# Optimization experiments

Hardware: AMD Instinct MI355X
Metric: run time of the kernel (lower is better)

## Reference

```python
import jax, jax.numpy as jnp
import numpy as np

EPS = 1e-5
HEADS, DIM_HEAD = 8, 64


def rmsnorm(x, g):
    # einn.Norm('b... [d]', mean=False, bias=False): rms-normalize last dim, learned scale
    return x * jax.lax.rsqrt(jnp.mean(jnp.square(x), axis=-1, keepdims=True) + EPS) * g


def setup_inputs() -> dict:
    key = jax.random.key(0)
    ks = jax.random.split(key, 10)
    B, N, D, DE, H, DH = 1, 1024, 512, 64, HEADS, DIM_HEAD
    s = 0.02
    return {
        'x': jax.random.normal(ks[0], (B, N, D), jnp.float32),
        'mask': jnp.ones((B, N), dtype=bool),
        'edges': jax.random.normal(ks[1], (B, N, N, DE), jnp.float32),
        'rms_g': jnp.ones((D,), jnp.float32),
        'w_qkv': jax.random.normal(ks[2], (D, 3 * H * DH), jnp.float32) * s,
        'w_gates': jax.random.normal(ks[3], (D, H), jnp.float32) * s,
        'b_gates': jnp.zeros((H,), jnp.float32),
        'edges_rms_g': jnp.ones((DE,), jnp.float32),
        'w_eb': jax.random.normal(ks[4], (DE, H), jnp.float32) * s,
        'b_eb': jnp.zeros((H,), jnp.float32),
        'w_th': jnp.eye(H, dtype=jnp.float32) + jax.random.normal(ks[5], (H, H), jnp.float32) * s,
        'w_out': jax.random.normal(ks[6], (H * DH, D), jnp.float32) * s,
        'w_eout': jax.random.normal(ks[7], (H, DE), jnp.float32) * s,
    }


def reference(x, mask, edges, rms_g, w_qkv, w_gates, b_gates, edges_rms_g, w_eb, b_eb, w_th, w_out, w_eout):
    B, N, D = x.shape
    H, DH = HEADS, DIM_HEAD
    scale = DH ** 0.5  # NOTE: source multiplies q by dim_head**0.5 (faithful)

    xn = rmsnorm(x, rms_g)
    qkv = (xn @ w_qkv).reshape(B, N, 3, H, DH)
    q = jnp.transpose(qkv[:, :, 0], (0, 2, 1, 3)) * scale  # b h n d
    k = jnp.transpose(qkv[:, :, 1], (0, 2, 1, 3))
    v = jnp.transpose(qkv[:, :, 2], (0, 2, 1, 3))

    sim = jnp.einsum('bhid,bhjd->bhij', q, k)
    # edge bias: rmsnorm -> Linear(dim_edges, heads) -> b h i j
    bias = jnp.einsum('bije,eh->bhij', rmsnorm(edges, edges_rms_g), w_eb) + b_eb[None, :, None, None]
    sim = sim + bias
    # pre talking heads: Conv2d(H, H, 1, bias=False)
    sim = jnp.einsum('bhij,gh->bgij', sim, w_th)

    mask_value = -jnp.finfo(sim.dtype).max
    sim = jnp.where(mask[:, None, None, :], sim, mask_value)

    attn = jax.nn.softmax(sim, axis=-1)
    out = jnp.einsum('bhij,bhjd->bhid', attn, v)

    gates = jax.nn.sigmoid(xn @ w_gates + b_gates)  # b n h
    out = out * jnp.transpose(gates, (0, 2, 1))[..., None]  # b h n 1

    out = jnp.transpose(out, (0, 2, 1, 3)).reshape(B, N, H * DH) @ w_out  # b n dim
    edges_out = jnp.einsum('bhij,he->bije', attn, w_eout)  # Conv2d(H, DE, 1) then b d i j -> b i j d
    return out, edges_out
```

## Files before the change

kernel.cpp:

```cpp
#include <hip/hip_runtime.h>
#include <math.h>

#define EPS 1e-5f

__global__ __launch_bounds__(256) void prep_kernel(
    const float* __restrict__ w_th, const float* __restrict__ w_eb,
    const float* __restrict__ b_eb, const float* __restrict__ erg,
    float* __restrict__ G2, float* __restrict__ b2)
{
  int t = threadIdx.x;
  for (int idx = t; idx < 512; idx += 256) {
    int g = idx >> 6, d = idx & 63;
    float s = 0.f;
#pragma unroll
    for (int h = 0; h < 8; ++h) s += w_th[g * 8 + h] * w_eb[d * 8 + h];
    G2[idx] = erg[d] * s;
  }
  if (t < 8) {
    float s = 0.f;
#pragma unroll
    for (int h = 0; h < 8; ++h) s += w_th[t * 8 + h] * b_eb[h];
    b2[t] = s;
  }
}

__global__ __launch_bounds__(256) void rms_gates_kernel(
    const float* __restrict__ x, const float* __restrict__ rms_g,
    const float* __restrict__ w_gates, const float* __restrict__ b_gates,
    float* __restrict__ xn, float* __restrict__ gates)
{
  int i = blockIdx.x, t = threadIdx.x;
  __shared__ float red[4][9];
  float2 v = *(const float2*)&x[i * 512 + t * 2];
  float g0 = rms_g[t * 2], g1 = rms_g[t * 2 + 1];
  float a0 = v.x * g0, a1 = v.y * g1;
  float ssq = v.x * v.x + v.y * v.y;
  float4 wa = *(const float4*)&w_gates[t * 16 + 0];
  float4 wb = *(const float4*)&w_gates[t * 16 + 4];
  float4 wc = *(const float4*)&w_gates[t * 16 + 8];
  float4 wd = *(const float4*)&w_gates[t * 16 + 12];
  float ph[8];
  ph[0] = a0 * wa.x + a1 * wc.x; ph[1] = a0 * wa.y + a1 * wc.y;
  ph[2] = a0 * wa.z + a1 * wc.z; ph[3] = a0 * wa.w + a1 * wc.w;
  ph[4] = a0 * wb.x + a1 * wd.x; ph[5] = a0 * wb.y + a1 * wd.y;
  ph[6] = a0 * wb.z + a1 * wd.z; ph[7] = a0 * wb.w + a1 * wd.w;
#pragma unroll
  for (int off = 32; off >= 1; off >>= 1) {
    ssq += __shfl_xor(ssq, off, 64);
#pragma unroll
    for (int h = 0; h < 8; ++h) ph[h] += __shfl_xor(ph[h], off, 64);
  }
  int wv = t >> 6;
  if ((t & 63) == 0) {
    red[wv][0] = ssq;
#pragma unroll
    for (int h = 0; h < 8; ++h) red[wv][1 + h] = ph[h];
  }
  __syncthreads();
  float ssqT = red[0][0] + red[1][0] + red[2][0] + red[3][0];
  float inv = rsqrtf(ssqT * (1.0f / 512.0f) + EPS);
  float2 o; o.x = v.x * inv * g0; o.y = v.y * inv * g1;
  *(float2*)&xn[i * 512 + t * 2] = o;
  if (t < 8) {
    float p = red[0][1 + t] + red[1][1 + t] + red[2][1 + t] + red[3][1 + t];
    float z = p * inv + b_gates[t];
    gates[i * 8 + t] = 1.0f / (1.0f + __expf(-z));
  }
}

__global__ __launch_bounds__(256) void gemm32_f32(
    const float* __restrict__ A, const float* __restrict__ B, float* __restrict__ C,
    int M, int N, int K)
{
  __shared__ float As[16][40];
  __shared__ float Bs[16][68];
  int t = threadIdx.x;
  int row0 = blockIdx.y * 32, col0 = blockIdx.x * 64;
  int tm = t & 7, tn = t >> 3;
  int ar = t >> 2, ac = (t & 3) * 4;
  int br = t >> 4, bc = (t & 15) * 4;
  float4 av, bv;
  if (t < 128) av = *(const float4*)&A[(size_t)(row0 + ar) * K + ac];
  bv = *(const float4*)&B[(size_t)br * N + col0 + bc];
  float acc[4][2] = {};
  for (int k0 = 0; k0 < K; k0 += 16) {
    __syncthreads();
    if (t < 128) {
      As[ac + 0][ar] = av.x; As[ac + 1][ar] = av.y; As[ac + 2][ar] = av.z; As[ac + 3][ar] = av.w;
    }
    *(float4*)&Bs[br][bc] = bv;
    __syncthreads();
    if (k0 + 16 < K) {
      if (t < 128) av = *(const float4*)&A[(size_t)(row0 + ar) * K + k0 + 16 + ac];
      bv = *(const float4*)&B[(size_t)(k0 + 16 + br) * N + col0 + bc];
    }
#pragma unroll
    for (int k = 0; k < 16; ++k) {
      float4 a = *(const float4*)&As[k][tm * 4];
      float2 b = *(const float2*)&Bs[k][tn * 2];
      acc[0][0] += a.x * b.x; acc[0][1] += a.x * b.y;
      acc[1][0] += a.y * b.x; acc[1][1] += a.y * b.y;
      acc[2][0] += a.z * b.x; acc[2][1] += a.z * b.y;
      acc[3][0] += a.w * b.x; acc[3][1] += a.w * b.y;
    }
  }
#pragma unroll
  for (int aa = 0; aa < 4; ++aa) {
    float2 o; o.x = acc[aa][0]; o.y = acc[aa][1];
    *(float2*)&C[(size_t)(row0 + tm * 4 + aa) * N + col0 + tn * 2] = o;
  }
}

__global__ __launch_bounds__(256) void qk_kernel(
    const float* __restrict__ qkv, float* __restrict__ sim)
{
  int jt = blockIdx.x, it = blockIdx.y, h = blockIdx.z;
  __shared__ float Qs[16][68];
  __shared__ float Ks[16][68];
  int t = threadIdx.x;
  int tm = t & 15, tn = t >> 4;
  int r = t >> 2, c4 = (t & 3) * 4;
  const float* qb = qkv + h * 64;
  const float* kb = qkv + 512 + h * 64;
  float4 qv = *(const float4*)&qb[(size_t)(it * 64 + r) * 1536 + c4];
  float4 kv = *(const float4*)&kb[(size_t)(jt * 64 + r) * 1536 + c4];
  float acc[4][4] = {};
  for (int k0 = 0; k0 < 64; k0 += 16) {
    __syncthreads();
    Qs[c4 + 0][r] = qv.x * 8.0f; Qs[c4 + 1][r] = qv.y * 8.0f; Qs[c4 + 2][r] = qv.z * 8.0f; Qs[c4 + 3][r] = qv.w * 8.0f;
    Ks[c4 + 0][r] = kv.x; Ks[c4 + 1][r] = kv.y; Ks[c4 + 2][r] = kv.z; Ks[c4 + 3][r] = kv.w;
    __syncthreads();
    if (k0 + 16 < 64) {
      qv = *(const float4*)&qb[(size_t)(it * 64 + r) * 1536 + k0 + 16 + c4];
      kv = *(const float4*)&kb[(size_t)(jt * 64 + r) * 1536 + k0 + 16 + c4];
    }
#pragma unroll
    for (int k = 0; k < 16; ++k) {
      float4 a = *(const float4*)&Qs[k][tm * 4];
      float4 b = *(const float4*)&Ks[k][tn * 4];
      acc[0][0] += a.x * b.x; acc[0][1] += a.x * b.y; acc[0][2] += a.x * b.z; acc[0][3] += a.x * b.w;
      acc[1][0] += a.y * b.x; acc[1][1] += a.y * b.y; acc[1][2] += a.y * b.z; acc[1][3] += a.y * b.w;
      acc[2][0] += a.z * b.x; acc[2][1] += a.z * b.y; acc[2][2] += a.z * b.z; acc[2][3] += a.z * b.w;
      acc[3][0] += a.w * b.x; acc[3][1] += a.w * b.y; acc[3][2] += a.w * b.z; acc[3][3] += a.w * b.w;
    }
  }
#pragma unroll
  for (int aa = 0; aa < 4; ++aa) {
    float4 o; o.x = acc[aa][0]; o.y = acc[aa][1]; o.z = acc[aa][2]; o.w = acc[aa][3];
    *(float4*)&sim[((size_t)h << 20) + (size_t)(it * 64 + tm * 4 + aa) * 1024 + jt * 64 + tn * 4] = o;
  }
}

__global__ __launch_bounds__(256) void attn_fused2(
    float* __restrict__ simattn,
    const float* __restrict__ edges,
    const float* __restrict__ w_th,
    const float* __restrict__ G2,
    const float* __restrict__ b2,
    const float* __restrict__ w_eout,
    float* __restrict__ edges_out)
{
  __shared__ float tile[256 * 17];
  __shared__ float red[4][8];
  int i = blockIdx.x, t = threadIdx.x;
  int wv = t >> 6;
  int sub = t & 15, grp = t >> 4;

  float weo[8][4];
#pragma unroll
  for (int g = 0; g < 8; ++g) {
    float4 v = *(const float4*)&w_eout[g * 64 + sub * 4];
    weo[g][0] = v.x; weo[g][1] = v.y; weo[g][2] = v.z; weo[g][3] = v.w;
  }
  float b2r[8];
#pragma unroll
  for (int g = 0; g < 8; ++g) b2r[g] = b2[g];

  const float* erow = edges + (size_t)i * 65536;
  float lgv[4][8];
  float vmax[8];
#pragma unroll
  for (int g = 0; g < 8; ++g) vmax[g] = -1e30f;

  float4 pf[4];
#pragma unroll
  for (int it = 0; it < 4; ++it) {
    int jr = (t >> 2) + 64 * it;
    pf[it] = *(const float4*)&erow[(size_t)jr * 64 + (t & 3) * 4];
  }

  for (int jg = 0; jg < 4; ++jg) {
    float ssq = 0.f;
    float dot[8] = {0.f, 0.f, 0.f, 0.f, 0.f, 0.f, 0.f, 0.f};
    for (int dc = 0; dc < 4; ++dc) {
      __syncthreads();
#pragma unroll
      for (int it = 0; it < 4; ++it) {
        int jr = (t >> 2) + 64 * it;
        float4 v = pf[it];
        tile[jr * 17 + (t & 3) * 4 + 0] = v.x;
        tile[jr * 17 + (t & 3) * 4 + 1] = v.y;
        tile[jr * 17 + (t & 3) * 4 + 2] = v.z;
        tile[jr * 17 + (t & 3) * 4 + 3] = v.w;
      }
      __syncthreads();
      {
        int ndc = dc + 1, njg = jg;
        if (ndc == 4) { ndc = 0; ++njg; }
        if (njg < 4) {
#pragma unroll
          for (int it = 0; it < 4; ++it) {
            int jr = (t >> 2) + 64 * it;
            pf[it] = *(const float4*)&erow[(size_t)(njg * 256 + jr) * 64 + ndc * 16 + (t & 3) * 4];
          }
        }
      }
#pragma unroll
      for (int d = 0; d < 16; ++d) {
        float e = tile[t * 17 + d];
        ssq += e * e;
        int dd = dc * 16 + d;
#pragma unroll
        for (int g = 0; g < 8; ++g) dot[g] += e * G2[g * 64 + dd];
      }
    }
    int j = jg * 256 + t;
    float l[8];
#pragma unroll
    for (int h = 0; h < 8; ++h) l[h] = simattn[((size_t)h << 20) + ((size_t)i << 10) + j];
    float r = rsqrtf(ssq * (1.0f / 64.0f) + EPS);
#pragma unroll
    for (int g = 0; g < 8; ++g) {
      float s = 0.f;
#pragma unroll
      for (int h = 0; h < 8; ++h) s += w_th[g * 8 + h] * l[h];
      s += dot[g] * r + b2r[g];
      lgv[jg][g] = s;
      vmax[g] = fmaxf(vmax[g], s);
    }
  }
#pragma unroll
  for (int g = 0; g < 8; ++g) {
#pragma unroll
    for (int off = 32; off >= 1; off >>= 1) vmax[g] = fmaxf(vmax[g], __shfl_xor(vmax[g], off, 64));
  }
  if ((t & 63) == 0) {
#pragma unroll
    for (int g = 0; g < 8; ++g) red[wv][g] = vmax[g];
  }
  __syncthreads();
  float mx[8];
#pragma unroll
  for (int g = 0; g < 8; ++g)
    mx[g] = fmaxf(fmaxf(red[0][g], red[1][g]), fmaxf(red[2][g], red[3][g]));
  __syncthreads();
  float vsum[8] = {0.f, 0.f, 0.f, 0.f, 0.f, 0.f, 0.f, 0.f};
#pragma unroll
  for (int jg = 0; jg < 4; ++jg) {
#pragma unroll
    for (int g = 0; g < 8; ++g) {
      float ev = __expf(lgv[jg][g] - mx[g]);
      lgv[jg][g] = ev;
      vsum[g] += ev;
    }
  }
#pragma unroll
  for (int g = 0; g < 8; ++g) {
#pragma unroll
    for (int off = 32; off >= 1; off >>= 1) vsum[g] += __shfl_xor(vsum[g], off, 64);
  }
  if ((t & 63) == 0) {
#pragma unroll
    for (int g = 0; g < 8; ++g) red[wv][g] = vsum[g];
  }
  __syncthreads();
  float inv[8];
#pragma unroll
  for (int g = 0; g < 8; ++g)
    inv[g] = 1.0f / (red[0][g] + red[1][g] + red[2][g] + red[3][g]);
#pragma unroll
  for (int jg = 0; jg < 4; ++jg) {
    int j = jg * 256 + t;
#pragma unroll
    for (int g = 0; g < 8; ++g) {
      float a = lgv[jg][g] * inv[g];
      lgv[jg][g] = a;
      simattn[((size_t)g << 20) + ((size_t)i << 10) + j] = a;
    }
  }
  float* lgc = tile;
  for (int jg = 0; jg < 4; ++jg) {
    __syncthreads();
#pragma unroll
    for (int g = 0; g < 8; ++g) lgc[g * 256 + t] = lgv[jg][g];
    __syncthreads();
#pragma unroll
    for (int pass = 0; pass < 16; ++pass) {
      int jj = pass * 16 + grp;
      float a[8];
#pragma unroll
      for (int g = 0; g < 8; ++g) a[g] = lgc[g * 256 + jj];
      float4 o;
      o.x = a[0] * weo[0][0]; o.y = a[0] * weo[0][1]; o.z = a[0] * weo[0][2]; o.w = a[0] * weo[0][3];
#pragma unroll
      for (int g = 1; g < 8; ++g) {
        o.x += a[g] * weo[g][0]; o.y += a[g] * weo[g][1];
        o.z += a[g] * weo[g][2]; o.w += a[g] * weo[g][3];
      }
      *(float4*)&edges_out[((size_t)(i * 1024 + jg * 256 + jj)) * 64 + sub * 4] = o;
    }
  }
}

__global__ __launch_bounds__(256) void av_kernel(
    const float* __restrict__ attn, const float* __restrict__ qkv,
    const float* __restrict__ gates, float* __restrict__ outh)
{
  int it = blockIdx.y, g = blockIdx.z;
  __shared__ float As[16][40];
  __shared__ float Bs[16][68];
  int t = threadIdx.x;
  int tm = t & 7, tn = t >> 3;
  int ar = t >> 2, ac = (t & 3) * 4;
  int br = t >> 4, bc = (t & 15) * 4;
  const float* Ab = attn + ((size_t)g << 20) + (size_t)(it * 32) * 1024;
  const float* Bb = qkv + 1024 + g * 64;
  float4 av, bv;
  if (t < 128) av = *(const float4*)&Ab[(size_t)ar * 1024 + ac];
  bv = *(const float4*)&Bb[(size_t)br * 1536 + bc];
  float acc[4][2] = {};
  for (int k0 = 0; k0 < 1024; k0 += 16) {
    __syncthreads();
    if (t < 128) {
      As[ac + 0][ar] = av.x; As[ac + 1][ar] = av.y; As[ac + 2][ar] = av.z; As[ac + 3][ar] = av.w;
    }
    *(float4*)&Bs[br][bc] = bv;
    __syncthreads();
    if (k0 + 16 < 1024) {
      if (t < 128) av = *(const float4*)&Ab[(size_t)ar * 1024 + k0 + 16 + ac];
      bv = *(const float4*)&Bb[(size_t)(k0 + 16 + br) * 1536 + bc];
    }
#pragma unroll
    for (int k = 0; k < 16; ++k) {
      float4 a = *(const float4*)&As[k][tm * 4];
      float2 b = *(const float2*)&Bs[k][tn * 2];
      acc[0][0] += a.x * b.x; acc[0][1] += a.x * b.y;
      acc[1][0] += a.y * b.x; acc[1][1] += a.y * b.y;
      acc[2][0] += a.z * b.x; acc[2][1] += a.z * b.y;
      acc[3][0] += a.w * b.x; acc[3][1] += a.w * b.y;
    }
  }
#pragma unroll
  for (int aa = 0; aa < 4; ++aa) {
    int irow = it * 32 + tm * 4 + aa;
    float gt = gates[irow * 8 + g];
    float2 o; o.x = acc[aa][0] * gt; o.y = acc[aa][1] * gt;
    *(float2*)&outh[(size_t)irow * 512 + g * 64 + tn * 2] = o;
  }
}

extern "C" void kernel_launch(void* const* d_in, const int* in_sizes, int n_in,
                              void* d_out, int out_size, void* d_ws, size_t ws_size,
                              hipStream_t stream) {
  const float* x       = (const float*)d_in[0];
  const float* edges   = (const float*)d_in[2];
  const float* rms_g   = (const float*)d_in[3];
  const float* w_qkv   = (const float*)d_in[4];
  const float* w_gates = (const float*)d_in[5];
  const float* b_gates = (const float*)d_in[6];
  const float* erg     = (const float*)d_in[7];
  const float* w_eb    = (const float*)d_in[8];
  const float* b_eb    = (const float*)d_in[9];
  const float* w_th    = (const float*)d_in[10];
  const float* w_out   = (const float*)d_in[11];
  const float* w_eout  = (const float*)d_in[12];

  float* out = (float*)d_out;
  float* eo  = out + 1024 * 512;

  float* ws    = (float*)d_ws;
  float* xn    = ws;
  float* gates = xn + 524288;
  float* qkv   = gates + 8192;
  float* sim   = qkv + 1572864;
  float* outh  = sim + 8388608;
  float* G2    = outh + 524288;
  float* b2    = G2 + 512;

  prep_kernel<<<1, 256, 0, stream>>>(w_th, w_eb, b_eb, erg, G2, b2);
  rms_gates_kernel<<<1024, 256, 0, stream>>>(x, rms_g, w_gates, b_gates, xn, gates);
  gemm32_f32<<<dim3(1536 / 64, 1024 / 32), 256, 0, stream>>>(xn, w_qkv, qkv, 1024, 1536, 512);
  qk_kernel<<<dim3(16, 16, 8), 256, 0, stream>>>(qkv, sim);
  attn_fused2<<<1024, 256, 0, stream>>>(sim, edges, w_th, G2, b2, w_eout, eo);
  av_kernel<<<dim3(1, 32, 8), 256, 0, stream>>>(sim, qkv, gates, outh);
  gemm32_f32<<<dim3(512 / 64, 1024 / 32), 256, 0, stream>>>(outh, w_out, out, 1024, 512, 512);
}
```

Measured before the change: 625.1 us.

## Split attn-V GEMM over key chunks, add 64x64 QKV GEMM, single-stage QK tile

The attention-times-V kernel previously launched only 256 blocks, each looping over all 1024 keys. It is now split into 8 key chunks that write partial sums to a workspace, followed by a reduction kernel that sums the partials and applies the sigmoid gates. The QKV projection switches to a new 64x64-tile GEMM, which gives more reuse per block but launches fewer blocks. The QK kernel now loads the full 64-wide head dimension into shared memory at once, removing the inner sync loop. In exchange this adds an extra partial-sum buffer, one more launch, and larger shared-memory use in the QK kernel.

```diff
diff --git a/kernel.cpp b/kernel.cpp
--- a/kernel.cpp
+++ b/kernel.cpp
@@ -111,38 +111,81 @@
   }
 }
 
+__global__ __launch_bounds__(256) void gemm64_f32(
+    const float* __restrict__ A, const float* __restrict__ B, float* __restrict__ C,
+    int M, int N, int K)
+{
+  __shared__ float As[16][68];
+  __shared__ float Bs[16][68];
+  int t = threadIdx.x;
+  int row0 = blockIdx.y * 64, col0 = blockIdx.x * 64;
+  int tm = t & 15, tn = t >> 4;
+  int ar = t >> 2, ac = (t & 3) * 4;
+  int br = t >> 4, bc = (t & 15) * 4;
+  float4 av = *(const float4*)&A[(size_t)(row0 + ar) * K + ac];
+  float4 bv = *(const float4*)&B[(size_t)br * N + col0 + bc];
+  float acc[4][4] = {};
+  for (int k0 = 0; k0 < K; k0 += 16) {
+    __syncthreads();
+    As[ac + 0][ar] = av.x; As[ac + 1][ar] = av.y; As[ac + 2][ar] = av.z; As[ac + 3][ar] = av.w;
+    *(float4*)&Bs[br][bc] = bv;
+    __syncthreads();
+    if (k0 + 16 < K) {
+      av = *(const float4*)&A[(size_t)(row0 + ar) * K + k0 + 16 + ac];
+      bv = *(const float4*)&B[(size_t)(k0 + 16 + br) * N + col0 + bc];
+    }
+#pragma unroll
+    for (int k = 0; k < 16; ++k) {
+      float4 a = *(const float4*)&As[k][tn * 4];
+      float4 b = *(const float4*)&Bs[k][tm * 4];
+      acc[0][0] += a.x * b.x; acc[0][1] += a.x * b.y; acc[0][2] += a.x * b.z; acc[0][3] += a.x * b.w;
+      acc[1][0] += a.y * b.x; acc[1][1] += a.y * b.y; acc[1][2] += a.y * b.z; acc[1][3] += a.y * b.w;
+      acc[2][0] += a.z * b.x; acc[2][1] += a.z * b.y; acc[2][2] += a.z * b.z; acc[2][3] += a.z * b.w;
+      acc[3][0] += a.w * b.x; acc[3][1] += a.w * b.y; acc[3][2] += a.w * b.z; acc[3][3] += a.w * b.w;
+    }
+  }
+#pragma unroll
+  for (int r = 0; r < 4; ++r) {
+    float4 o; o.x = acc[r][0]; o.y = acc[r][1]; o.z = acc[r][2]; o.w = acc[r][3];
+    *(float4*)&C[(size_t)(row0 + tn * 4 + r) * N + col0 + tm * 4] = o;
+  }
+}
+
 __global__ __launch_bounds__(256) void qk_kernel(
     const float* __restrict__ qkv, float* __restrict__ sim)
 {
   int jt = blockIdx.x, it = blockIdx.y, h = blockIdx.z;
-  __shared__ float Qs[16][68];
-  __shared__ float Ks[16][68];
+  __shared__ float Qs[64][68];
+  __shared__ float Ks[64][68];
   int t = threadIdx.x;
   int tm = t & 15, tn = t >> 4;
   int r = t >> 2, c4 = (t & 3) * 4;
   const float* qb = qkv + h * 64;
   const float* kb = qkv + 512 + h * 64;
-  float4 qv = *(const float4*)&qb[(size_t)(it * 64 + r) * 1536 + c4];
-  float4 kv = *(const float4*)&kb[(size_t)(jt * 64 + r) * 1536 + c4];
+  float4 qv[4], kv[4];
+#pragma unroll
+  for (int ch = 0; ch < 4; ++ch) {
+    qv[ch] = *(const float4*)&qb[(size_t)(it * 64 + r) * 1536 + ch * 16 + c4];
+    kv[ch] = *(const float4*)&kb[(size_t)(jt * 64 + r) * 1536 + ch * 16 + c4];
+  }
+#pragma unroll
+  for (int ch = 0; ch < 4; ++ch) {
+    int d0 = ch * 16 + c4;
+    Qs[d0 + 0][r] = qv[ch].x * 8.0f; Qs[d0 + 1][r] = qv[ch].y * 8.0f;
+    Qs[d0 + 2][r] = qv[ch].z * 8.0f; Qs[d0 + 3][r] = qv[ch].w * 8.0f;
+    Ks[d0 + 0][r] = kv[ch].x; Ks[d0 + 1][r] = kv[ch].y;
+    Ks[d0 + 2][r] = kv[ch].z; Ks[d0 + 3][r] = kv[ch].w;
+  }
+  __syncthreads();
   float acc[4][4] = {};
-  for (int k0 = 0; k0 < 64; k0 += 16) {
-    __syncthreads();
-    Qs[c4 + 0][r] = qv.x * 8.0f; Qs[c4 + 1][r] = qv.y * 8.0f; Qs[c4 + 2][r] = qv.z * 8.0f; Qs[c4 + 3][r] = qv.w * 8.0f;
-    Ks[c4 + 0][r] = kv.x; Ks[c4 + 1][r] = kv.y; Ks[c4 + 2][r] = kv.z; Ks[c4 + 3][r] = kv.w;
-    __syncthreads();
-    if (k0 + 16 < 64) {
-      qv = *(const float4*)&qb[(size_t)(it * 64 + r) * 1536 + k0 + 16 + c4];
-      kv = *(const float4*)&kb[(size_t)(jt * 64 + r) * 1536 + k0 + 16 + c4];
-    }
-#pragma unroll
-    for (int k = 0; k < 16; ++k) {
-      float4 a = *(const float4*)&Qs[k][tm * 4];
-      float4 b = *(const float4*)&Ks[k][tn * 4];
-      acc[0][0] += a.x * b.x; acc[0][1] += a.x * b.y; acc[0][2] += a.x * b.z; acc[0][3] += a.x * b.w;
-      acc[1][0] += a.y * b.x; acc[1][1] += a.y * b.y; acc[1][2] += a.y * b.z; acc[1][3] += a.y * b.w;
-      acc[2][0] += a.z * b.x; acc[2][1] += a.z * b.y; acc[2][2] += a.z * b.z; acc[2][3] += a.z * b.w;
-      acc[3][0] += a.w * b.x; acc[3][1] += a.w * b.y; acc[3][2] += a.w * b.z; acc[3][3] += a.w * b.w;
-    }
+#pragma unroll
+  for (int k = 0; k < 64; ++k) {
+    float4 a = *(const float4*)&Qs[k][tm * 4];
+    float4 b = *(const float4*)&Ks[k][tn * 4];
+    acc[0][0] += a.x * b.x; acc[0][1] += a.x * b.y; acc[0][2] += a.x * b.z; acc[0][3] += a.x * b.w;
+    acc[1][0] += a.y * b.x; acc[1][1] += a.y * b.y; acc[1][2] += a.y * b.z; acc[1][3] += a.y * b.w;
+    acc[2][0] += a.z * b.x; acc[2][1] += a.z * b.y; acc[2][2] += a.z * b.z; acc[2][3] += a.z * b.w;
+    acc[3][0] += a.w * b.x; acc[3][1] += a.w * b.y; acc[3][2] += a.w * b.z; acc[3][3] += a.w * b.w;
   }
 #pragma unroll
   for (int aa = 0; aa < 4; ++aa) {
@@ -312,31 +355,31 @@
   }
 }
 
-__global__ __launch_bounds__(256) void av_kernel(
+__global__ __launch_bounds__(256) void av_part(
     const float* __restrict__ attn, const float* __restrict__ qkv,
-    const float* __restrict__ gates, float* __restrict__ outh)
-{
-  int it = blockIdx.y, g = blockIdx.z;
+    float* __restrict__ outp)
+{
+  int jc = blockIdx.x, it = blockIdx.y, g = blockIdx.z;
   __shared__ float As[16][40];
   __shared__ float Bs[16][68];
   int t = threadIdx.x;
   int tm = t & 7, tn = t >> 3;
   int ar = t >> 2, ac = (t & 3) * 4;
   int br = t >> 4, bc = (t & 15) * 4;
-  const float* Ab = attn + ((size_t)g << 20) + (size_t)(it * 32) * 1024;
-  const float* Bb = qkv + 1024 + g * 64;
+  const float* Ab = attn + ((size_t)g << 20) + (size_t)(it * 32) * 1024 + jc * 128;
+  const float* Bb = qkv + 1024 + g * 64 + (size_t)(jc * 128) * 1536;
   float4 av, bv;
   if (t < 128) av = *(const float4*)&Ab[(size_t)ar * 1024 + ac];
   bv = *(const float4*)&Bb[(size_t)br * 1536 + bc];
   float acc[4][2] = {};
-  for (int k0 = 0; k0 < 1024; k0 += 16) {
+  for (int k0 = 0; k0 < 128; k0 += 16) {
     __syncthreads();
     if (t < 128) {
       As[ac + 0][ar] = av.x; As[ac + 1][ar] = av.y; As[ac + 2][ar] = av.z; As[ac + 3][ar] = av.w;
     }
     *(float4*)&Bs[br][bc] = bv;
     __syncthreads();
-    if (k0 + 16 < 1024) {
+    if (k0 + 16 < 128) {
       if (t < 128) av = *(const float4*)&Ab[(size_t)ar * 1024 + k0 + 16 + ac];
       bv = *(const float4*)&Bb[(size_t)(k0 + 16 + br) * 1536 + bc];
     }
@@ -353,10 +396,26 @@
 #pragma unroll
   for (int aa = 0; aa < 4; ++aa) {
     int irow = it * 32 + tm * 4 + aa;
-    float gt = gates[irow * 8 + g];
-    float2 o; o.x = acc[aa][0] * gt; o.y = acc[aa][1] * gt;
-    *(float2*)&outh[(size_t)irow * 512 + g * 64 + tn * 2] = o;
-  }
+    float2 o; o.x = acc[aa][0]; o.y = acc[aa][1];
+    *(float2*)&outp[((size_t)jc * 1024 + irow) * 512 + g * 64 + tn * 2] = o;
+  }
+}
+
+__global__ __launch_bounds__(256) void av_reduce(
+    const float* __restrict__ outp, const float* __restrict__ gates,
+    float* __restrict__ outh)
+{
+  int i = blockIdx.x, t = threadIdx.x;
+  int c = t * 2;
+  float2 s = *(const float2*)&outp[(size_t)i * 512 + c];
+#pragma unroll
+  for (int jc = 1; jc < 8; ++jc) {
+    float2 p = *(const float2*)&outp[((size_t)jc * 1024 + i) * 512 + c];
+    s.x += p.x; s.y += p.y;
+  }
+  float gt = gates[i * 8 + (c >> 6)];
+  s.x *= gt; s.y *= gt;
+  *(float2*)&outh[(size_t)i * 512 + c] = s;
 }
 
 extern "C" void kernel_launch(void* const* d_in, const int* in_sizes, int n_in,
@@ -386,12 +445,14 @@
   float* outh  = sim + 8388608;
   float* G2    = outh + 524288;
   float* b2    = G2 + 512;
+  float* outp  = b2 + 8;
 
   prep_kernel<<<1, 256, 0, stream>>>(w_th, w_eb, b_eb, erg, G2, b2);
   rms_gates_kernel<<<1024, 256, 0, stream>>>(x, rms_g, w_gates, b_gates, xn, gates);
-  gemm32_f32<<<dim3(1536 / 64, 1024 / 32), 256, 0, stream>>>(xn, w_qkv, qkv, 1024, 1536, 512);
+  gemm64_f32<<<dim3(1536 / 64, 1024 / 64), 256, 0, stream>>>(xn, w_qkv, qkv, 1024, 1536, 512);
   qk_kernel<<<dim3(16, 16, 8), 256, 0, stream>>>(qkv, sim);
   attn_fused2<<<1024, 256, 0, stream>>>(sim, edges, w_th, G2, b2, w_eout, eo);
-  av_kernel<<<dim3(1, 32, 8), 256, 0, stream>>>(sim, qkv, gates, outh);
+  av_part<<<dim3(8, 32, 8), 256, 0, stream>>>(sim, qkv, outp);
+  av_reduce<<<1024, 256, 0, stream>>>(outp, gates, outh);
   gemm32_f32<<<dim3(512 / 64, 1024 / 32), 256, 0, stream>>>(outh, w_out, out, 1024, 512, 512);
 }
```

New measurement: 614.8 us. No clear change (-1.6%).
